# Performance work log

Measured on AMD Instinct MI355X. Metric: run time of the kernel, lower is better.

Reference implementation:

```python
import jax, jax.numpy as jnp
import numpy as np
import math

N = 4264          # all_node_num
B = 256           # batch size
VIS = 784 + 50    # input_node_num + label_node_num
NG = 8            # number of color groups (Pegasus chromatic number is small)
GS = N // NG      # 533 nodes per group
SAMPLE_NUM = 10   # Gibbs sweeps (default 1000 in source; reduced for reference)
AVG_DEG = 15.0    # Pegasus graph degree ~15


def setup_inputs() -> dict:
    key = jax.random.key(0)
    k1, k2, k3, k4 = jax.random.split(key, 4)
    # spin state in {-1, +1}, shape [B, N]
    m = jnp.where(jax.random.normal(k1, (B, N)) >= 0, 1.0, -1.0).astype(jnp.float32)
    # sparse symmetric coupling matrix J: ~AVG_DEG neighbors per node, values randn*0.01
    upper_mask = jnp.triu(jax.random.uniform(k2, (N, N)) < (AVG_DEG / N), k=1)
    Jup = jax.random.normal(k3, (N, N), dtype=jnp.float32) * 0.01 * upper_mask
    J = Jup + Jup.T
    # bias H: log-odds constant on visible nodes, zero on hidden
    h_vis = math.log((VIS / N) / (1.0 - VIS / N))
    H = jnp.zeros((N,), dtype=jnp.float32).at[:VIS].set(h_vis)
    # color groups: disjoint partition of node indices, [NG, GS]
    groups = jax.random.permutation(k4, N).reshape(NG, GS).astype(jnp.int32)
    return {"m": m, "J": J, "H": H, "groups": groups, "sample_num": SAMPLE_NUM}


def reference(m, J, H, groups, sample_num):
    n_groups = groups.shape[0]

    def sweep(m, key):
        keys = jax.random.split(key, n_groups)
        for g in range(n_groups):          # small fixed set of color groups
            idx = groups[g]                # [GS]
            # I = sparse.mm(J[idx], m.T).T + H[idx]  ->  [B, GS]
            I = jnp.einsum('bn,gn->bg', m, J[idx]) + H[idx]
            r = jax.random.uniform(keys[g], I.shape, dtype=I.dtype) * 2.0 - 1.0
            m = m.at[:, idx].set(jnp.sign(jnp.tanh(I) - r))
        return m, None

    iter_keys = jax.random.split(jax.random.key(42), sample_num)
    m, _ = jax.lax.scan(sweep, m, iter_keys)
    return m
```

## Files before the change

### kernel.cpp

```cpp
#include <hip/hip_runtime.h>
#include <hip/hip_bf16.h>
#include <stdint.h>

#define NN 4264
#define BB 256
#define GSZ 533
#define NGRP 8
#define NSWEEP 10
#define NSTEP (NSWEEP * NGRP)
#define DMAX 48
#define NCOLD 24
#define NHOT 12
#define NPACK 36
#define NF4 1066
#define NIT 17

struct Keys { unsigned k0[NSTEP]; unsigned k1[NSTEP]; };

#define TF_ROUND(x0, x1, r) { x0 += x1; x1 = (x1 << (r)) | (x1 >> (32 - (r))); x1 ^= x0; }
#define TF_BODY(K0, K1, C0, C1, O0, O1) {                                   \
  unsigned ks0 = (K0), ks1 = (K1), ks2 = (K0) ^ (K1) ^ 0x1BD11BDAu;          \
  unsigned x0 = (C0) + ks0, x1 = (C1) + ks1;                                 \
  TF_ROUND(x0, x1, 13) TF_ROUND(x0, x1, 15) TF_ROUND(x0, x1, 26) TF_ROUND(x0, x1, 6)  \
  x0 += ks1; x1 += ks2 + 1u;                                                 \
  TF_ROUND(x0, x1, 17) TF_ROUND(x0, x1, 29) TF_ROUND(x0, x1, 16) TF_ROUND(x0, x1, 24) \
  x0 += ks2; x1 += ks0 + 2u;                                                 \
  TF_ROUND(x0, x1, 13) TF_ROUND(x0, x1, 15) TF_ROUND(x0, x1, 26) TF_ROUND(x0, x1, 6)  \
  x0 += ks0; x1 += ks1 + 3u;                                                 \
  TF_ROUND(x0, x1, 17) TF_ROUND(x0, x1, 29) TF_ROUND(x0, x1, 16) TF_ROUND(x0, x1, 24) \
  x0 += ks1; x1 += ks2 + 4u;                                                 \
  TF_ROUND(x0, x1, 13) TF_ROUND(x0, x1, 15) TF_ROUND(x0, x1, 26) TF_ROUND(x0, x1, 6)  \
  x0 += ks2; x1 += ks0 + 5u;                                                 \
  (O0) = x0; (O1) = x1; }

static void tf_host(unsigned k0, unsigned k1, unsigned c0, unsigned c1,
                    unsigned* o0, unsigned* o1) {
  unsigned a, b;
  TF_BODY(k0, k1, c0, c1, a, b);
  *o0 = a; *o1 = b;
}

__device__ __forceinline__ void tf_dev(unsigned k0, unsigned k1, unsigned c0, unsigned c1,
                                       unsigned& o0, unsigned& o1) {
  TF_BODY(k0, k1, c0, c1, o0, o1);
}

__device__ __forceinline__ float tf_r(unsigned k0, unsigned k1, unsigned c) {
  unsigned o0, o1;
  tf_dev(k0, k1, 0u, c, o0, o1);
  const unsigned bits = o0 ^ o1;
  const float u = __uint_as_float((bits >> 9) | 0x3f800000u) - 1.0f;
  return u * 2.0f - 1.0f;
}

__global__ __launch_bounds__(256) void build_inv(const int* __restrict__ groups,
                                                 int* __restrict__ invg) {
  const int p = blockIdx.x * 256 + threadIdx.x;
  if (p < NN) invg[groups[p]] = p / GSZ;
}

__global__ __launch_bounds__(256) void build_ell(const float* __restrict__ J,
                                                 const int* __restrict__ groups,
                                                 const int* __restrict__ invg,
                                                 unsigned* __restrict__ pack,
                                                 int2* __restrict__ exact8,
                                                 int* __restrict__ deg,
                                                 float* __restrict__ marg) {
  __shared__ int2 scr[4][DMAX];
  const int wv = threadIdx.x >> 6, lane = threadIdx.x & 63;
  const int p = blockIdx.x * 4 + wv;
  if (p >= NN) return;
  const int node = groups[p];
  const int prevg = (p / GSZ + NGRP - 1) % NGRP;
  const float4* row = (const float4*)(J + (size_t)node * NN);

  float4 vv[NIT];
#pragma unroll
  for (int it = 0; it < NIT; ++it) {
    const int q = it * 64 + lane;
    vv[it] = (q < NF4) ? row[q] : make_float4(0.0f, 0.0f, 0.0f, 0.0f);
  }

  int cnt = 0;
#pragma unroll
  for (int it = 0; it < NIT; ++it) {
    const float4 v = vv[it];
    const int c0 = (it * 64 + lane) * 4;
#define COMP(X, CIDX) {                                                        \
      const bool nz = ((X) != 0.0f);                                           \
      const unsigned long long mk = __ballot(nz);                              \
      const int rk = cnt + __popcll(mk & ((1ull << lane) - 1ull));             \
      if (nz && rk < DMAX) {                                                   \
        const int2 e = make_int2((CIDX), __float_as_int(X));                   \
        exact8[(size_t)p * DMAX + rk] = e;                                     \
        scr[wv][rk] = e;                                                       \
      }                                                                        \
      cnt += __popcll(mk); }
    COMP(v.x, c0 + 0) COMP(v.y, c0 + 1) COMP(v.z, c0 + 2) COMP(v.w, c0 + 3)
#undef COMP
  }

  const int cl = (cnt < DMAX) ? cnt : DMAX;
  const bool vl = (lane < cl);
  int col = 0; float val = 0.0f;
  if (vl) { const int2 e = scr[wv][lane]; col = e.x; val = __int_as_float(e.y); }
  const bool hot = vl && (invg[col] == prevg);
  const unsigned long long hm = __ballot(hot);
  const int nH = __popcll(hm);
  const int rkH = __popcll(hm & ((1ull << lane) - 1ull));
  const bool bad = (cnt > NPACK) || (nH > NHOT);
  float asum = vl ? fabsf(val) : 0.0f;

  if (!bad) {
    if (vl) {
      const int rkC = lane - rkH;
      const int slot = hot ? (NCOLD + rkH)
                           : ((rkC < NCOLD) ? rkC : nH + rkC);
      const unsigned bits = __float_as_uint(val);
      const unsigned bf = (bits + 0x7fffu + ((bits >> 16) & 1u)) >> 16;
      pack[(size_t)p * NPACK + slot] = (bf << 16) | ((unsigned)col << 2);
    }
    const int nC = cl - nH;
    const int cend = (nC < NCOLD) ? nC : NCOLD;
    const int hend = (nC > NCOLD) ? cl : (NCOLD + nH);
    for (int k = lane; k < NPACK; k += 64)
      if ((k >= cend && k < NCOLD) || (k >= hend))
        pack[(size_t)p * NPACK + k] = 0u;
  } else {
    for (int k = lane; k < NPACK; k += 64) pack[(size_t)p * NPACK + k] = 0u;
  }

  for (int s = 1; s < 64; s <<= 1) asum += __shfl_xor(asum, s, 64);
  if (lane == 0) {
    deg[p] = cl;
    marg[p] = bad ? 1e30f : (asum * 0.001953125f + 2e-5f);
  }
}

__global__ __launch_bounds__(576, 3) void gibbs(const float* __restrict__ m0,
                                                const float* __restrict__ H,
                                                const int* __restrict__ groups,
                                                const unsigned* __restrict__ pack,
                                                const int2* __restrict__ exact8,
                                                const int* __restrict__ deg,
                                                const float* __restrict__ marg,
                                                float* __restrict__ out,
                                                Keys keys) {
  __shared__ float m_lds[NN];
  const int b = blockIdx.x;
  const int i = threadIdx.x;
  const bool active = (i < GSZ);

  for (int n = i; n < NN; n += 576) m_lds[n] = m0[(size_t)b * NN + n];

  int nodeg[NGRP];
  float hg[NGRP], mgg[NGRP];
  int dgg[NGRP];
  if (active) {
#pragma unroll
    for (int g = 0; g < NGRP; ++g) {
      const int p = g * GSZ + i;
      nodeg[g] = groups[p];
      hg[g] = H[nodeg[g]];
      dgg[g] = deg[p];
      mgg[g] = marg[p];
    }
  }

  const unsigned c = (unsigned)(b * GSZ + i);

#define MV(W)  (*(const float*)((const char*)m_lds + ((W) & 0xFFFCu)))
#define ACC4(W, A0, A1, A2, A3)                                   \
  A0 += __uint_as_float((W).x & 0xFFFF0000u) * MV((W).x);         \
  A1 += __uint_as_float((W).y & 0xFFFF0000u) * MV((W).y);         \
  A2 += __uint_as_float((W).z & 0xFFFF0000u) * MV((W).z);         \
  A3 += __uint_as_float((W).w & 0xFFFF0000u) * MV((W).w);

  uint4 h0, h1, h2;
  uint4 p0, p1, p2, p3, p4, p5;
  float preSum = 0.0f, rcur = 0.0f;

  if (active) {
    const uint4* q0 = (const uint4*)(pack + (size_t)i * NPACK);
    p0 = q0[0]; p1 = q0[1]; p2 = q0[2]; p3 = q0[3]; p4 = q0[4]; p5 = q0[5];
    h0 = q0[6]; h1 = q0[7]; h2 = q0[8];
    rcur = tf_r(keys.k0[0], keys.k1[0], c);
  }
  __syncthreads();
  if (active) {
    float a0 = 0.0f, a1 = 0.0f, a2 = 0.0f, a3 = 0.0f;
    ACC4(p0, a0, a1, a2, a3) ACC4(p1, a0, a1, a2, a3) ACC4(p2, a0, a1, a2, a3)
    ACC4(p3, a0, a1, a2, a3) ACC4(p4, a0, a1, a2, a3) ACC4(p5, a0, a1, a2, a3)
    preSum = (a0 + a1) + (a2 + a3);
  }

#pragma unroll 1
  for (int t = 0; t < NSWEEP; ++t) {
#pragma unroll
    for (int g = 0; g < NGRP; ++g) {
      const int step = t * NGRP + g;
      float nv = 0.0f;
      uint4 n6, n7, n8;
      float rnext = 0.0f, npre = 0.0f;
      if (active) {
        const int gn = (g + 1) & (NGRP - 1);
        const uint4* qn = (const uint4*)(pack + (size_t)(gn * GSZ + i) * NPACK);
        const uint4 n0 = qn[0], n1 = qn[1], n2 = qn[2];
        const uint4 n3 = qn[3], n4 = qn[4], n5 = qn[5];
        n6 = qn[6]; n7 = qn[7]; n8 = qn[8];

        const int sn = (step + 1 < NSTEP) ? step + 1 : step;
        rnext = tf_r(keys.k0[sn], keys.k1[sn], c);

        float a0 = 0.0f, a1 = 0.0f, a2 = 0.0f, a3 = 0.0f;
        ACC4(h0, a0, a1, a2, a3) ACC4(h1, a0, a1, a2, a3) ACC4(h2, a0, a1, a2, a3)

        float b0 = 0.0f, b1 = 0.0f, b2 = 0.0f, b3 = 0.0f;
        ACC4(n0, b0, b1, b2, b3) ACC4(n1, b0, b1, b2, b3) ACC4(n2, b0, b1, b2, b3)
        ACC4(n3, b0, b1, b2, b3) ACC4(n4, b0, b1, b2, b3) ACC4(n5, b0, b1, b2, b3)
        npre = (b0 + b1) + (b2 + b3);

        const float I = preSum + ((a0 + a1) + (a2 + a3)) + hg[g];
        const float th = tanhf(I);
        const float d = th - rcur;
        if (__builtin_expect(fabsf(d) > mgg[g], 1)) {
          nv = (d > 0.0f) ? 1.0f : -1.0f;
        } else {
          const int dg = dgg[g];
          const int2* ep = exact8 + (size_t)(g * GSZ + i) * DMAX;
          double I64 = (double)hg[g];
          for (int k = 0; k < dg; ++k) {
            const int2 e = ep[k];
            I64 += (double)__int_as_float(e.y) * (double)m_lds[e.x];
          }
          const double diff = tanh(I64) - (double)rcur;
          nv = (diff > 0.0) ? 1.0f : ((diff < 0.0) ? -1.0f : 0.0f);
        }
      }
      __syncthreads();
      if (active) m_lds[nodeg[g]] = nv;
      __syncthreads();
      if (active) {
        preSum = npre; rcur = rnext;
        h0 = n6; h1 = n7; h2 = n8;
      }
    }
  }

  for (int n = i; n < NN; n += 576) out[(size_t)b * NN + n] = m_lds[n];
#undef ACC4
#undef MV
}

extern "C" void kernel_launch(void* const* d_in, const int* in_sizes, int n_in,
                              void* d_out, int out_size, void* d_ws, size_t ws_size,
                              hipStream_t stream) {
  const float* m0     = (const float*)d_in[0];
  const float* J      = (const float*)d_in[1];
  const float* H      = (const float*)d_in[2];
  const int*   groups = (const int*)d_in[3];

  char* ws = (char*)d_ws;
  unsigned* pack   = (unsigned*)ws;                     ws += (size_t)NN * NPACK * 4;
  int2*     exact8 = (int2*)ws;                         ws += (size_t)NN * DMAX * 8;
  int*      deg    = (int*)ws;                          ws += (size_t)NN * 4;
  float*    marg   = (float*)ws;                        ws += (size_t)NN * 4;
  int*      invg   = (int*)ws;

  Keys keys;
  for (int t = 0; t < NSWEEP; ++t) {
    unsigned ik0, ik1;
    tf_host(0u, 42u, 0u, (unsigned)t, &ik0, &ik1);
    for (int g = 0; g < NGRP; ++g) {
      unsigned gk0, gk1;
      tf_host(ik0, ik1, 0u, (unsigned)g, &gk0, &gk1);
      keys.k0[t * NGRP + g] = gk0;
      keys.k1[t * NGRP + g] = gk1;
    }
  }

  build_inv<<<(NN + 255) / 256, 256, 0, stream>>>(groups, invg);
  build_ell<<<(NN + 3) / 4, 256, 0, stream>>>(J, groups, invg, pack, exact8, deg, marg);
  gibbs<<<BB, 576, 0, stream>>>(m0, H, groups, pack, exact8, deg, marg,
                                (float*)d_out, keys);
}
```

Baseline: 337.3 us.

## Shrink packed ELL rows, stream per-group node metadata, compute RNG keys on device

Cuts the cold neighbor slots from 24 to 20, so each packed row is 32 words and the next-group prefetch carries fewer uint4 registers. The per-thread arrays of node index, bias, margin and degree for all eight groups are replaced by one int4 aux record that is prefetched each step. The Threefry step keys move from a host-side kernel argument to a small device kernel whose output is staged in LDS. Together these lower register pressure in the Gibbs kernel and drop the launch-bounds occupancy hint. Rows with more than 20 cold neighbors now depend on the slow fallback or spill layout, and there is one extra kernel launch.

```diff
diff --git a/kernel.cpp b/kernel.cpp
--- a/kernel.cpp
+++ b/kernel.cpp
@@ -9,13 +9,11 @@
 #define NSWEEP 10
 #define NSTEP (NSWEEP * NGRP)
 #define DMAX 48
-#define NCOLD 24
+#define NCOLD 20
 #define NHOT 12
-#define NPACK 36
+#define NPACK 32
 #define NF4 1066
 #define NIT 17
-
-struct Keys { unsigned k0[NSTEP]; unsigned k1[NSTEP]; };
 
 #define TF_ROUND(x0, x1, r) { x0 += x1; x1 = (x1 << (r)) | (x1 >> (32 - (r))); x1 ^= x0; }
 #define TF_BODY(K0, K1, C0, C1, O0, O1) {                                   \
@@ -33,13 +31,6 @@
   x0 += ks2; x1 += ks0 + 5u;                                                 \
   (O0) = x0; (O1) = x1; }
 
-static void tf_host(unsigned k0, unsigned k1, unsigned c0, unsigned c1,
-                    unsigned* o0, unsigned* o1) {
-  unsigned a, b;
-  TF_BODY(k0, k1, c0, c1, a, b);
-  *o0 = a; *o1 = b;
-}
-
 __device__ __forceinline__ void tf_dev(unsigned k0, unsigned k1, unsigned c0, unsigned c1,
                                        unsigned& o0, unsigned& o1) {
   TF_BODY(k0, k1, c0, c1, o0, o1);
@@ -53,6 +44,17 @@
   return u * 2.0f - 1.0f;
 }
 
+__global__ __launch_bounds__(128) void build_keys(unsigned* __restrict__ kk) {
+  const int s = threadIdx.x;
+  if (s < NSTEP) {
+    unsigned ik0, ik1, gk0, gk1;
+    tf_dev(0u, 42u, 0u, (unsigned)(s / NGRP), ik0, ik1);
+    tf_dev(ik0, ik1, 0u, (unsigned)(s & (NGRP - 1)), gk0, gk1);
+    kk[2 * s] = gk0;
+    kk[2 * s + 1] = gk1;
+  }
+}
+
 __global__ __launch_bounds__(256) void build_inv(const int* __restrict__ groups,
                                                  int* __restrict__ invg) {
   const int p = blockIdx.x * 256 + threadIdx.x;
@@ -60,12 +62,12 @@
 }
 
 __global__ __launch_bounds__(256) void build_ell(const float* __restrict__ J,
+                                                 const float* __restrict__ H,
                                                  const int* __restrict__ groups,
                                                  const int* __restrict__ invg,
                                                  unsigned* __restrict__ pack,
                                                  int2* __restrict__ exact8,
-                                                 int* __restrict__ deg,
-                                                 float* __restrict__ marg) {
+                                                 int4* __restrict__ aux) {
   __shared__ int2 scr[4][DMAX];
   const int wv = threadIdx.x >> 6, lane = threadIdx.x & 63;
   const int p = blockIdx.x * 4 + wv;
@@ -132,40 +134,25 @@
 
   for (int s = 1; s < 64; s <<= 1) asum += __shfl_xor(asum, s, 64);
   if (lane == 0) {
-    deg[p] = cl;
-    marg[p] = bad ? 1e30f : (asum * 0.001953125f + 2e-5f);
-  }
-}
-
-__global__ __launch_bounds__(576, 3) void gibbs(const float* __restrict__ m0,
-                                                const float* __restrict__ H,
-                                                const int* __restrict__ groups,
-                                                const unsigned* __restrict__ pack,
-                                                const int2* __restrict__ exact8,
-                                                const int* __restrict__ deg,
-                                                const float* __restrict__ marg,
-                                                float* __restrict__ out,
-                                                Keys keys) {
+    const float mval = bad ? 1e30f : (asum * 0.001953125f + 2e-5f);
+    aux[p] = make_int4(node, __float_as_int(H[node]), __float_as_int(mval), cl);
+  }
+}
+
+__global__ __launch_bounds__(576) void gibbs(const float* __restrict__ m0,
+                                             const unsigned* __restrict__ pack,
+                                             const int2* __restrict__ exact8,
+                                             const int4* __restrict__ aux,
+                                             const unsigned* __restrict__ keys,
+                                             float* __restrict__ out) {
   __shared__ float m_lds[NN];
+  __shared__ unsigned k_lds[2 * NSTEP];
   const int b = blockIdx.x;
   const int i = threadIdx.x;
   const bool active = (i < GSZ);
 
   for (int n = i; n < NN; n += 576) m_lds[n] = m0[(size_t)b * NN + n];
-
-  int nodeg[NGRP];
-  float hg[NGRP], mgg[NGRP];
-  int dgg[NGRP];
-  if (active) {
-#pragma unroll
-    for (int g = 0; g < NGRP; ++g) {
-      const int p = g * GSZ + i;
-      nodeg[g] = groups[p];
-      hg[g] = H[nodeg[g]];
-      dgg[g] = deg[p];
-      mgg[g] = marg[p];
-    }
-  }
+  if (i < 2 * NSTEP) k_lds[i] = keys[i];
 
   const unsigned c = (unsigned)(b * GSZ + i);
 
@@ -177,20 +164,22 @@
   A3 += __uint_as_float((W).w & 0xFFFF0000u) * MV((W).w);
 
   uint4 h0, h1, h2;
-  uint4 p0, p1, p2, p3, p4, p5;
+  int4 acur;
   float preSum = 0.0f, rcur = 0.0f;
 
+  uint4 w0, w1, w2, w3, w4;
   if (active) {
     const uint4* q0 = (const uint4*)(pack + (size_t)i * NPACK);
-    p0 = q0[0]; p1 = q0[1]; p2 = q0[2]; p3 = q0[3]; p4 = q0[4]; p5 = q0[5];
-    h0 = q0[6]; h1 = q0[7]; h2 = q0[8];
-    rcur = tf_r(keys.k0[0], keys.k1[0], c);
+    w0 = q0[0]; w1 = q0[1]; w2 = q0[2]; w3 = q0[3]; w4 = q0[4];
+    h0 = q0[5]; h1 = q0[6]; h2 = q0[7];
+    acur = aux[i];
   }
   __syncthreads();
   if (active) {
+    rcur = tf_r(k_lds[0], k_lds[1], c);
     float a0 = 0.0f, a1 = 0.0f, a2 = 0.0f, a3 = 0.0f;
-    ACC4(p0, a0, a1, a2, a3) ACC4(p1, a0, a1, a2, a3) ACC4(p2, a0, a1, a2, a3)
-    ACC4(p3, a0, a1, a2, a3) ACC4(p4, a0, a1, a2, a3) ACC4(p5, a0, a1, a2, a3)
+    ACC4(w0, a0, a1, a2, a3) ACC4(w1, a0, a1, a2, a3) ACC4(w2, a0, a1, a2, a3)
+    ACC4(w3, a0, a1, a2, a3) ACC4(w4, a0, a1, a2, a3)
     preSum = (a0 + a1) + (a2 + a3);
   }
 
@@ -200,35 +189,38 @@
     for (int g = 0; g < NGRP; ++g) {
       const int step = t * NGRP + g;
       float nv = 0.0f;
-      uint4 n6, n7, n8;
+      uint4 n5, n6, n7;
+      int4 anext;
       float rnext = 0.0f, npre = 0.0f;
       if (active) {
         const int gn = (g + 1) & (NGRP - 1);
-        const uint4* qn = (const uint4*)(pack + (size_t)(gn * GSZ + i) * NPACK);
+        const int pn = gn * GSZ + i;
+        const uint4* qn = (const uint4*)(pack + (size_t)pn * NPACK);
         const uint4 n0 = qn[0], n1 = qn[1], n2 = qn[2];
-        const uint4 n3 = qn[3], n4 = qn[4], n5 = qn[5];
-        n6 = qn[6]; n7 = qn[7]; n8 = qn[8];
+        const uint4 n3 = qn[3], n4 = qn[4];
+        n5 = qn[5]; n6 = qn[6]; n7 = qn[7];
+        anext = aux[pn];
 
         const int sn = (step + 1 < NSTEP) ? step + 1 : step;
-        rnext = tf_r(keys.k0[sn], keys.k1[sn], c);
+        rnext = tf_r(k_lds[2 * sn], k_lds[2 * sn + 1], c);
 
         float a0 = 0.0f, a1 = 0.0f, a2 = 0.0f, a3 = 0.0f;
         ACC4(h0, a0, a1, a2, a3) ACC4(h1, a0, a1, a2, a3) ACC4(h2, a0, a1, a2, a3)
 
         float b0 = 0.0f, b1 = 0.0f, b2 = 0.0f, b3 = 0.0f;
         ACC4(n0, b0, b1, b2, b3) ACC4(n1, b0, b1, b2, b3) ACC4(n2, b0, b1, b2, b3)
-        ACC4(n3, b0, b1, b2, b3) ACC4(n4, b0, b1, b2, b3) ACC4(n5, b0, b1, b2, b3)
+        ACC4(n3, b0, b1, b2, b3) ACC4(n4, b0, b1, b2, b3)
         npre = (b0 + b1) + (b2 + b3);
 
-        const float I = preSum + ((a0 + a1) + (a2 + a3)) + hg[g];
+        const float I = preSum + ((a0 + a1) + (a2 + a3)) + __int_as_float(acur.y);
         const float th = tanhf(I);
         const float d = th - rcur;
-        if (__builtin_expect(fabsf(d) > mgg[g], 1)) {
+        if (__builtin_expect(fabsf(d) > __int_as_float(acur.z), 1)) {
           nv = (d > 0.0f) ? 1.0f : -1.0f;
         } else {
-          const int dg = dgg[g];
+          const int dg = acur.w;
           const int2* ep = exact8 + (size_t)(g * GSZ + i) * DMAX;
-          double I64 = (double)hg[g];
+          double I64 = (double)__int_as_float(acur.y);
           for (int k = 0; k < dg; ++k) {
             const int2 e = ep[k];
             I64 += (double)__int_as_float(e.y) * (double)m_lds[e.x];
@@ -238,11 +230,12 @@
         }
       }
       __syncthreads();
-      if (active) m_lds[nodeg[g]] = nv;
+      if (active) m_lds[acur.x] = nv;
       __syncthreads();
       if (active) {
         preSum = npre; rcur = rnext;
-        h0 = n6; h1 = n7; h2 = n8;
+        h0 = n5; h1 = n6; h2 = n7;
+        acur = anext;
       }
     }
   }
@@ -263,24 +256,12 @@
   char* ws = (char*)d_ws;
   unsigned* pack   = (unsigned*)ws;                     ws += (size_t)NN * NPACK * 4;
   int2*     exact8 = (int2*)ws;                         ws += (size_t)NN * DMAX * 8;
-  int*      deg    = (int*)ws;                          ws += (size_t)NN * 4;
-  float*    marg   = (float*)ws;                        ws += (size_t)NN * 4;
-  int*      invg   = (int*)ws;
-
-  Keys keys;
-  for (int t = 0; t < NSWEEP; ++t) {
-    unsigned ik0, ik1;
-    tf_host(0u, 42u, 0u, (unsigned)t, &ik0, &ik1);
-    for (int g = 0; g < NGRP; ++g) {
-      unsigned gk0, gk1;
-      tf_host(ik0, ik1, 0u, (unsigned)g, &gk0, &gk1);
-      keys.k0[t * NGRP + g] = gk0;
-      keys.k1[t * NGRP + g] = gk1;
-    }
-  }
-
+  int4*     aux    = (int4*)ws;                         ws += (size_t)NN * 16;
+  int*      invg   = (int*)ws;                          ws += (size_t)NN * 4;
+  unsigned* keys   = (unsigned*)ws;
+
+  build_keys<<<1, 128, 0, stream>>>(keys);
   build_inv<<<(NN + 255) / 256, 256, 0, stream>>>(groups, invg);
-  build_ell<<<(NN + 3) / 4, 256, 0, stream>>>(J, groups, invg, pack, exact8, deg, marg);
-  gibbs<<<BB, 576, 0, stream>>>(m0, H, groups, pack, exact8, deg, marg,
-                                (float*)d_out, keys);
-}
+  build_ell<<<(NN + 3) / 4, 256, 0, stream>>>(J, H, groups, invg, pack, exact8, aux);
+  gibbs<<<BB, 576, 0, stream>>>(m0, pack, exact8, aux, keys, (float*)d_out);
+}
```

Measured after the change: 353.9 us. 4.9% more time.
